# Kernel optimization log

Hardware: AMD Instinct MI355X
Metric: run time of the kernel (lower is better)

Reference implementation:

```python
import jax, jax.numpy as jnp
import numpy as np

N_DST = 50000
NUM_HEAD = 2
LN_EPS = 1e-5


def setup_inputs() -> dict:
    key = jax.random.key(0)
    ks = jax.random.split(key, 12)
    n_dst, n_src, E = 50000, 200000, 250000
    dim_node, dim_edge, dim_time, dim_out = 128, 64, 64, 128
    d_q = dim_node + dim_time            # w_q input dim
    d_k = dim_node + dim_edge + dim_time  # w_k / w_v input dim
    d_o = dim_node + dim_out              # w_out input dim
    f32 = jnp.float32
    return {
        "h": jax.random.normal(ks[0], (n_dst + n_src, dim_node), f32),
        "dt": jax.random.uniform(ks[1], (E,), f32) * 100.0,
        "ef": jax.random.normal(ks[2], (E, dim_edge), f32),
        # TimeEncode: cos(t * w + b), classic TGAT init w = 1/10^linspace(0,9)
        "time_w": (1.0 / 10.0 ** jnp.linspace(0.0, 9.0, dim_time)).astype(f32),
        "time_b": jnp.zeros((dim_time,), f32),
        "wq_w": (jax.random.normal(ks[3], (d_q, dim_out), f32) / np.sqrt(d_q)),
        "wq_b": jnp.zeros((dim_out,), f32),
        "wk_w": (jax.random.normal(ks[4], (d_k, dim_out), f32) / np.sqrt(d_k)),
        "wk_b": jnp.zeros((dim_out,), f32),
        "wv_w": (jax.random.normal(ks[5], (d_k, dim_out), f32) / np.sqrt(d_k)),
        "wv_b": jnp.zeros((dim_out,), f32),
        "wo_w": (jax.random.normal(ks[6], (d_o, dim_out), f32) / np.sqrt(d_o)),
        "wo_b": jnp.zeros((dim_out,), f32),
        "ln_g": jnp.ones((dim_out,), f32),
        "ln_b": jnp.zeros((dim_out,), f32),
        "nbr_idx": jax.random.randint(ks[7], (E,), 0, n_src),
        "edge_dst": jax.random.randint(ks[8], (E,), 0, n_dst),
    }


def reference(h, dt, ef, time_w, time_b, wq_w, wq_b, wk_w, wk_b, wv_w, wv_b,
              wo_w, wo_b, ln_g, ln_b, nbr_idx, edge_dst):
    n_dst = N_DST
    H = NUM_HEAD
    h_dst = h[:n_dst]                       # [n_dst, D]
    h_src = h[n_dst:]                       # [n_src, D]

    # time encoding: cos(t * w + b)
    time_feat = jnp.cos(dt[:, None] * time_w + time_b)          # [E, Dt]
    zero_time = jnp.broadcast_to(jnp.cos(time_b), (n_dst, time_b.shape[0]))

    Q_in = jnp.concatenate([h_dst, zero_time], axis=1)           # [n_dst, D+Dt]
    K_in = jnp.concatenate([h_src[nbr_idx], ef, time_feat], axis=1)  # [E, D+De+Dt]

    Q = (Q_in @ wq_w + wq_b)[edge_dst]      # [E, dim_out] gathered per edge
    K = K_in @ wk_w + wk_b                  # [E, dim_out]
    V = K_in @ wv_w + wv_b                  # [E, dim_out]

    E_ = Q.shape[0]
    Qh = Q.reshape(E_, H, -1)
    Kh = K.reshape(E_, H, -1)
    Vh = V.reshape(E_, H, -1)

    att_raw = jax.nn.leaky_relu(jnp.sum(Qh * Kh, axis=2), 0.2)   # [E, H]

    # edge_softmax: segment softmax over incoming edges of each dst node
    m = jax.ops.segment_max(att_raw, edge_dst, num_segments=n_dst)
    m = jnp.where(jnp.isfinite(m), m, 0.0)  # guard empty segments
    ex = jnp.exp(att_raw - m[edge_dst])
    den = jax.ops.segment_sum(ex, edge_dst, num_segments=n_dst)
    att = ex / den[edge_dst]                # [E, H]

    Vw = (Vh * att[..., None]).reshape(E_, -1)                   # [E, dim_out]
    agg = jax.ops.segment_sum(Vw, edge_dst, num_segments=n_dst)  # [n_dst, dim_out]

    pre = jax.nn.relu(jnp.concatenate([agg, h_dst], axis=1) @ wo_w + wo_b)
    mu = jnp.mean(pre, axis=-1, keepdims=True)
    var = jnp.var(pre, axis=-1, keepdims=True)
    return (pre - mu) / jnp.sqrt(var + LN_EPS) * ln_g + ln_b
```

## Files before the change

### kernel.cpp

```cpp
#include <hip/hip_runtime.h>
#include <hip/hip_bf16.h>
#include <math.h>


using bf16 = __hip_bfloat16;
typedef __attribute__((ext_vector_type(8))) short short8;
typedef __attribute__((ext_vector_type(4))) float f32x4;

static __device__ __forceinline__ unsigned short bf16_bits(float x) {
    bf16 h = __float2bfloat16(x);
    unsigned short b;
    __builtin_memcpy(&b, &h, 2);
    return b;
}
static __device__ __forceinline__ unsigned pk2(float x, float y) {
    return (unsigned)bf16_bits(x) | ((unsigned)bf16_bits(y) << 16);
}
static __device__ __forceinline__ float bflo(unsigned u) {
    return __uint_as_float(u << 16);
}
static __device__ __forceinline__ float bfhi(unsigned u) {
    return __uint_as_float(u & 0xffff0000u);
}
union frag_u { short8 s; unsigned u[4]; };

__global__ void k_pack(unsigned short* wkT, unsigned short* wvT, unsigned short* woT,
                       unsigned short* wqhT, unsigned short* wqlT, float* qbias,
                       const float* __restrict__ wk_w, const float* __restrict__ wv_w,
                       const float* __restrict__ wo_w, const float* __restrict__ wq_w,
                       const float* __restrict__ wq_b, const float* __restrict__ time_b) {
    int idx = blockIdx.x * blockDim.x + threadIdx.x;
    if (idx < 32768) {
        int n = idx >> 8, k = idx & 255;
        wkT[idx] = bf16_bits(wk_w[(size_t)k * 128 + n]);
        wvT[idx] = bf16_bits(wv_w[(size_t)k * 128 + n]);
        woT[idx] = bf16_bits(wo_w[(size_t)k * 128 + n]);
        if (idx < 16384) {
            int n2 = idx >> 7, k2 = idx & 127;
            float v = wq_w[(size_t)k2 * 128 + n2];
            unsigned short hb = bf16_bits(v);
            wqhT[idx] = hb;
            wqlT[idx] = bf16_bits(v - __uint_as_float((unsigned)hb << 16));
        }
        if (idx < 128) {
            float s = wq_b[idx];
            for (int j = 0; j < 64; ++j)
                s += cosf(time_b[j]) * wq_w[(128 + j) * 128 + idx];
            qbias[idx] = s;
        }
    }
}

__global__ void k_count(const int* __restrict__ edst, int* cnt, int E) {
    int e = blockIdx.x * 256 + threadIdx.x;
    if (e < E) atomicAdd(&cnt[edst[e]], 1);
}

__global__ void k_scan1(const int* __restrict__ cnt, int* rs, int* bsum, int n) {
    __shared__ int s[256];
    int t = threadIdx.x;
    int i = blockIdx.x * 256 + t;
    int v = (i < n) ? cnt[i] : 0;
    s[t] = v;
    __syncthreads();
    for (int off = 1; off < 256; off <<= 1) {
        int x = (t >= off) ? s[t - off] : 0;
        __syncthreads();
        s[t] += x;
        __syncthreads();
    }
    if (i < n) rs[i] = s[t] - v;
    if (t == 255) bsum[blockIdx.x] = s[255];
}

__global__ void k_scan2(int* bsum, int nblk) {
    __shared__ int s[256];
    int t = threadIdx.x;
    int v = (t < nblk) ? bsum[t] : 0;
    s[t] = v;
    __syncthreads();
    for (int off = 1; off < 256; off <<= 1) {
        int x = (t >= off) ? s[t - off] : 0;
        __syncthreads();
        s[t] += x;
        __syncthreads();
    }
    if (t < nblk) bsum[t] = s[t] - v;
}

__global__ void k_scatter(const int* __restrict__ edst, const int* __restrict__ rs,
                          const int* __restrict__ bsum, int* fill, int* epos, int E) {
    int e = blockIdx.x * 256 + threadIdx.x;
    if (e < E) {
        int d = edst[e];
        epos[e] = rs[d] + bsum[d >> 8] + atomicAdd(&fill[d], 1);
    }
}

__global__ __launch_bounds__(512) void k_q(
    float* __restrict__ Q, const float* __restrict__ h,
    const unsigned short* __restrict__ wqhT, const unsigned short* __restrict__ wqlT,
    const float* __restrict__ qbias, int ndst)
{
    __shared__ unsigned short Bs[32768];
    int tid = threadIdx.x;
    int lane = tid & 63, l15 = lane & 15, lk = lane >> 4;
    int r0 = blockIdx.x * 128 + (tid >> 6) * 16;
    int ra = r0 + l15;
    int rc = (ra < ndst) ? ra : (ndst - 1);
    const float* hrow = h + (size_t)rc * 128;

    float4 hx[4][2];
    #pragma unroll
    for (int kk = 0; kk < 4; ++kk) {
        int c0 = kk * 32 + lk * 8;
        hx[kk][0] = *reinterpret_cast<const float4*>(hrow + c0);
        hx[kk][1] = *reinterpret_cast<const float4*>(hrow + c0 + 4);
    }

    #pragma unroll
    for (int it = 0; it < 4; ++it) {
        int i = it * 512 + tid;
        int row = i >> 4, c = i & 15;
        int sw = ((c ^ (row & 15)) << 3);
        uint4 v = *reinterpret_cast<const uint4*>(wqhT + (size_t)row * 128 + c * 8);
        *reinterpret_cast<uint4*>(Bs + row * 128 + sw) = v;
        uint4 w = *reinterpret_cast<const uint4*>(wqlT + (size_t)row * 128 + c * 8);
        *reinterpret_cast<uint4*>(Bs + 16384 + row * 128 + sw) = w;
    }

    frag_u ah[4], al[4];
    #pragma unroll
    for (int kk = 0; kk < 4; ++kk) {
        float xs[8] = {hx[kk][0].x, hx[kk][0].y, hx[kk][0].z, hx[kk][0].w,
                       hx[kk][1].x, hx[kk][1].y, hx[kk][1].z, hx[kk][1].w};
        unsigned short hb[8];
        float lo[8];
        #pragma unroll
        for (int t = 0; t < 8; ++t) {
            hb[t] = bf16_bits(xs[t]);
            lo[t] = xs[t] - __uint_as_float((unsigned)hb[t] << 16);
        }
        #pragma unroll
        for (int t = 0; t < 4; ++t)
            ah[kk].u[t] = (unsigned)hb[2*t] | ((unsigned)hb[2*t+1] << 16);
        al[kk].u[0] = pk2(lo[0], lo[1]); al[kk].u[1] = pk2(lo[2], lo[3]);
        al[kk].u[2] = pk2(lo[4], lo[5]); al[kk].u[3] = pk2(lo[6], lo[7]);
    }

    f32x4 ck[8];
    #pragma unroll
    for (int nt = 0; nt < 8; ++nt) ck[nt] = (f32x4){0.f, 0.f, 0.f, 0.f};

    __syncthreads();
    #pragma unroll
    for (int kk2 = 0; kk2 < 4; ++kk2) {
        int co = ((kk2 * 4 + lk) ^ l15) << 3;
        #pragma unroll
        for (int nt = 0; nt < 8; ++nt) {
            int ro = (nt * 16 + l15) * 128;
            short8 bh = *reinterpret_cast<const short8*>(Bs + ro + co);
            short8 bl = *reinterpret_cast<const short8*>(Bs + 16384 + ro + co);
            ck[nt] = __builtin_amdgcn_mfma_f32_16x16x32_bf16(ah[kk2].s, bh, ck[nt], 0, 0, 0);
            ck[nt] = __builtin_amdgcn_mfma_f32_16x16x32_bf16(al[kk2].s, bh, ck[nt], 0, 0, 0);
            ck[nt] = __builtin_amdgcn_mfma_f32_16x16x32_bf16(ah[kk2].s, bl, ck[nt], 0, 0, 0);
        }
    }

    #pragma unroll
    for (int nt = 0; nt < 8; ++nt) {
        int col = nt * 16 + l15;
        float qb = qbias[col];
        #pragma unroll
        for (int j = 0; j < 4; ++j) {
            int row = r0 + lk * 4 + j;
            if (row < ndst) Q[(size_t)row * 128 + col] = ck[nt][j] + qb;
        }
    }
}

__global__ __launch_bounds__(512) void k_kvA(
    const float* __restrict__ h, const int* __restrict__ nbr, const int* __restrict__ edst,
    const float* __restrict__ dt, const float* __restrict__ ef,
    const float* __restrict__ time_w, const float* __restrict__ time_b,
    const unsigned short* __restrict__ wkT, const unsigned short* __restrict__ wvT,
    const float* __restrict__ wk_b, const float* __restrict__ Q,
    const int* __restrict__ epos,
    unsigned short* __restrict__ Vbuf, float2* __restrict__ att2, int ndst, int E)
{
    __shared__ unsigned short Bs[32768];
    int tid  = threadIdx.x;
    int lane = tid & 63;
    int l15  = lane & 15;
    int lk   = lane >> 4;
    int e0   = blockIdx.x * 128 + (tid >> 6) * 16;

    int  ea = e0 + l15;
    bool va = ea < E;
    int  na = va ? nbr[ea] : 0;
    float da = va ? dt[ea] : 0.f;
    const float* hrow = h + (size_t)(ndst + na) * 128;
    const float* erow = ef + (size_t)ea * 64;

    int dstr[4], pe[4];
    bool evv[4];
    #pragma unroll
    for (int j = 0; j < 4; ++j) {
        int ed = e0 + lk * 4 + j;
        evv[j]  = ed < E;
        dstr[j] = evv[j] ? edst[ed] : 0;
        pe[j]   = evv[j] ? epos[ed] : 0;
    }

    float4 hx[4][2], ex_[2][2];
    const float4 z4 = make_float4(0.f, 0.f, 0.f, 0.f);
    #pragma unroll
    for (int kk = 0; kk < 4; ++kk) {
        int c0 = kk * 32 + lk * 8;
        hx[kk][0] = va ? *reinterpret_cast<const float4*>(hrow + c0)     : z4;
        hx[kk][1] = va ? *reinterpret_cast<const float4*>(hrow + c0 + 4) : z4;
    }
    #pragma unroll
    for (int t = 0; t < 2; ++t) {
        int c = (4 + t) * 32 + lk * 8 - 128;
        ex_[t][0] = va ? *reinterpret_cast<const float4*>(erow + c)     : z4;
        ex_[t][1] = va ? *reinterpret_cast<const float4*>(erow + c + 4) : z4;
    }

    float qg[8][4];
    #pragma unroll
    for (int nt = 0; nt < 8; ++nt) {
        int gc = nt * 16 + l15;
        #pragma unroll
        for (int j = 0; j < 4; ++j)
            qg[nt][j] = Q[(size_t)dstr[j] * 128 + gc];
    }

    #pragma unroll
    for (int it = 0; it < 8; ++it) {
        int i = it * 512 + tid;
        int row = i >> 5, c = i & 31;
        uint4 v = *reinterpret_cast<const uint4*>(wkT + (size_t)row * 256 + c * 8);
        *reinterpret_cast<uint4*>(Bs + row * 256 + ((c ^ (row & 15)) << 3)) = v;
    }

    float tf[16];
    {
        int j0 = lk * 8;
        #pragma unroll
        for (int t = 0; t < 8; ++t) tf[t]     = __cosf(fmaf(da, time_w[j0 + t],      time_b[j0 + t]));
        #pragma unroll
        for (int t = 0; t < 8; ++t) tf[8 + t] = __cosf(fmaf(da, time_w[j0 + 32 + t], time_b[j0 + 32 + t]));
    }

    frag_u a[8];
    #pragma unroll
    for (int kk = 0; kk < 4; ++kk) {
        a[kk].u[0] = pk2(hx[kk][0].x, hx[kk][0].y); a[kk].u[1] = pk2(hx[kk][0].z, hx[kk][0].w);
        a[kk].u[2] = pk2(hx[kk][1].x, hx[kk][1].y); a[kk].u[3] = pk2(hx[kk][1].z, hx[kk][1].w);
    }
    #pragma unroll
    for (int t = 0; t < 2; ++t) {
        a[4+t].u[0] = pk2(ex_[t][0].x, ex_[t][0].y); a[4+t].u[1] = pk2(ex_[t][0].z, ex_[t][0].w);
        a[4+t].u[2] = pk2(ex_[t][1].x, ex_[t][1].y); a[4+t].u[3] = pk2(ex_[t][1].z, ex_[t][1].w);
    }
    a[6].u[0] = pk2(tf[0], tf[1]);  a[6].u[1] = pk2(tf[2], tf[3]);
    a[6].u[2] = pk2(tf[4], tf[5]);  a[6].u[3] = pk2(tf[6], tf[7]);
    a[7].u[0] = pk2(tf[8], tf[9]);  a[7].u[1] = pk2(tf[10], tf[11]);
    a[7].u[2] = pk2(tf[12], tf[13]); a[7].u[3] = pk2(tf[14], tf[15]);

    f32x4 ck[8];
    #pragma unroll
    for (int nt = 0; nt < 8; ++nt) ck[nt] = (f32x4){0.f, 0.f, 0.f, 0.f};

    __syncthreads();
    #pragma unroll
    for (int kk2 = 0; kk2 < 8; ++kk2) {
        int co = ((kk2 * 4 + lk) ^ l15) << 3;
        #pragma unroll
        for (int nt = 0; nt < 8; ++nt) {
            short8 b = *reinterpret_cast<const short8*>(Bs + (nt * 16 + l15) * 256 + co);
            ck[nt] = __builtin_amdgcn_mfma_f32_16x16x32_bf16(a[kk2].s, b, ck[nt], 0, 0, 0);
        }
    }
    __syncthreads();
    #pragma unroll
    for (int it = 0; it < 8; ++it) {
        int i = it * 512 + tid;
        int row = i >> 5, c = i & 31;
        uint4 v = *reinterpret_cast<const uint4*>(wvT + (size_t)row * 256 + c * 8);
        *reinterpret_cast<uint4*>(Bs + row * 256 + ((c ^ (row & 15)) << 3)) = v;
    }

    float p0[4], p1[4];
    #pragma unroll
    for (int j = 0; j < 4; ++j) { p0[j] = 0.f; p1[j] = 0.f; }
    #pragma unroll
    for (int nt = 0; nt < 8; ++nt) {
        float kb = wk_b[nt * 16 + l15];
        #pragma unroll
        for (int j = 0; j < 4; ++j) {
            float t = (ck[nt][j] + kb) * qg[nt][j];
            if (nt < 4) p0[j] += t; else p1[j] += t;
        }
    }
    #pragma unroll
    for (int m = 1; m <= 8; m <<= 1)
        #pragma unroll
        for (int j = 0; j < 4; ++j) {
            p0[j] += __shfl_xor(p0[j], m, 64);
            p1[j] += __shfl_xor(p1[j], m, 64);
        }
    if (l15 == 0) {
        #pragma unroll
        for (int j = 0; j < 4; ++j)
            if (evv[j]) {
                float r0 = p0[j]; r0 = (r0 >= 0.f) ? r0 : 0.2f * r0;
                float r1 = p1[j]; r1 = (r1 >= 0.f) ? r1 : 0.2f * r1;
                att2[pe[j]] = make_float2(r0, r1);
            }
    }

    f32x4 cv[8];
    #pragma unroll
    for (int nt = 0; nt < 8; ++nt) cv[nt] = (f32x4){0.f, 0.f, 0.f, 0.f};
    __syncthreads();
    #pragma unroll
    for (int kk2 = 0; kk2 < 8; ++kk2) {
        int co = ((kk2 * 4 + lk) ^ l15) << 3;
        #pragma unroll
        for (int nt = 0; nt < 8; ++nt) {
            short8 b = *reinterpret_cast<const short8*>(Bs + (nt * 16 + l15) * 256 + co);
            cv[nt] = __builtin_amdgcn_mfma_f32_16x16x32_bf16(a[kk2].s, b, cv[nt], 0, 0, 0);
        }
    }

    #pragma unroll
    for (int j = 0; j < 4; ++j)
        if (evv[j]) {
            uint4 val;
            val.x = pk2(cv[0][j], cv[1][j]);
            val.y = pk2(cv[2][j], cv[3][j]);
            val.z = pk2(cv[4][j], cv[5][j]);
            val.w = pk2(cv[6][j], cv[7][j]);
            *reinterpret_cast<uint4*>(Vbuf + (size_t)pe[j] * 128 + l15 * 8) = val;
        }
}

__global__ __launch_bounds__(256) void k_agg(
    const unsigned short* __restrict__ Vbuf, const float2* __restrict__ att2,
    const int* __restrict__ rs, const int* __restrict__ bsum, const int* __restrict__ cnt,
    const float* __restrict__ wv_b, float* __restrict__ agg, int ndst)
{
    int w = threadIdx.x >> 6, lane = threadIdx.x & 63;
    int d = blockIdx.x * 4 + w;
    if (d >= ndst) return;
    int p0 = lane * 2, p1 = p0 + 1;
    int c0 = ((p0 & 7) << 4) + (p0 >> 3);
    int c1 = ((p1 & 7) << 4) + (p1 >> 3);
    bool h0 = (p0 & 4) != 0, h1 = (p1 & 4) != 0;
    int base = rs[d] + bsum[d >> 8], n = cnt[d];
    const unsigned* V32 = reinterpret_cast<const unsigned*>(Vbuf);
    float den0 = 0.f, den1 = 0.f, acc0 = 0.f, acc1 = 0.f;
    int i = 0;
    for (; i + 4 <= n; i += 4) {
        size_t r = (size_t)(base + i);
        float2 a0 = att2[r], a1 = att2[r+1], a2 = att2[r+2], a3 = att2[r+3];
        unsigned w0 = V32[r*64 + lane], w1 = V32[(r+1)*64 + lane];
        unsigned w2 = V32[(r+2)*64 + lane], w3 = V32[(r+3)*64 + lane];
        float e00 = __expf(a0.x), e01 = __expf(a0.y);
        float e10 = __expf(a1.x), e11 = __expf(a1.y);
        float e20 = __expf(a2.x), e21 = __expf(a2.y);
        float e30 = __expf(a3.x), e31 = __expf(a3.y);
        den0 += e00 + e10 + e20 + e30;
        den1 += e01 + e11 + e21 + e31;
        acc0 = fmaf(h0 ? e01 : e00, bflo(w0), acc0);
        acc1 = fmaf(h1 ? e01 : e00, bfhi(w0), acc1);
        acc0 = fmaf(h0 ? e11 : e10, bflo(w1), acc0);
        acc1 = fmaf(h1 ? e11 : e10, bfhi(w1), acc1);
        acc0 = fmaf(h0 ? e21 : e20, bflo(w2), acc0);
        acc1 = fmaf(h1 ? e21 : e20, bfhi(w2), acc1);
        acc0 = fmaf(h0 ? e31 : e30, bflo(w3), acc0);
        acc1 = fmaf(h1 ? e31 : e30, bfhi(w3), acc1);
    }
    for (; i < n; ++i) {
        size_t r = (size_t)(base + i);
        float2 at = att2[r];
        float ex0 = __expf(at.x), ex1 = __expf(at.y);
        den0 += ex0; den1 += ex1;
        unsigned vv = V32[r*64 + lane];
        acc0 = fmaf(h0 ? ex1 : ex0, bflo(vv), acc0);
        acc1 = fmaf(h1 ? ex1 : ex0, bfhi(vv), acc1);
    }
    float o0 = 0.f, o1 = 0.f;
    if (n > 0) {
        o0 = acc0 / (h0 ? den1 : den0) + wv_b[c0];
        o1 = acc1 / (h1 ? den1 : den0) + wv_b[c1];
    }
    agg[(size_t)d * 128 + c0] = o0;
    agg[(size_t)d * 128 + c1] = o1;
}

__global__ __launch_bounds__(512) void k_out(
    const float* __restrict__ agg, const float* __restrict__ h,
    const unsigned short* __restrict__ woT, const float* __restrict__ wo_b,
    const float* __restrict__ ln_g, const float* __restrict__ ln_b,
    float* __restrict__ out, int ndst)
{
    __shared__ unsigned short Bs[32768];
    int tid = threadIdx.x;
    int lane = tid & 63, l15 = lane & 15, lk = lane >> 4;
    int r0 = blockIdx.x * 128 + (tid >> 6) * 16;
    int ra = r0 + l15;
    int rc = (ra < ndst) ? ra : (ndst - 1);
    const float* arow = agg + (size_t)rc * 128;
    const float* hrow = h + (size_t)rc * 128;

    float4 ax[4][2], hx[4][2];
    #pragma unroll
    for (int kk = 0; kk < 4; ++kk) {
        int c0 = kk * 32 + lk * 8;
        ax[kk][0] = *reinterpret_cast<const float4*>(arow + c0);
        ax[kk][1] = *reinterpret_cast<const float4*>(arow + c0 + 4);
        hx[kk][0] = *reinterpret_cast<const float4*>(hrow + c0);
        hx[kk][1] = *reinterpret_cast<const float4*>(hrow + c0 + 4);
    }

    #pragma unroll
    for (int it = 0; it < 8; ++it) {
        int i = it * 512 + tid;
        int row = i >> 5, c = i & 31;
        uint4 v = *reinterpret_cast<const uint4*>(woT + (size_t)row * 256 + c * 8);
        *reinterpret_cast<uint4*>(Bs + row * 256 + ((c ^ (row & 15)) << 3)) = v;
    }

    frag_u aa[4], ah[4];
    #pragma unroll
    for (int kk = 0; kk < 4; ++kk) {
        aa[kk].u[0] = pk2(ax[kk][0].x, ax[kk][0].y); aa[kk].u[1] = pk2(ax[kk][0].z, ax[kk][0].w);
        aa[kk].u[2] = pk2(ax[kk][1].x, ax[kk][1].y); aa[kk].u[3] = pk2(ax[kk][1].z, ax[kk][1].w);
        ah[kk].u[0] = pk2(hx[kk][0].x, hx[kk][0].y); ah[kk].u[1] = pk2(hx[kk][0].z, hx[kk][0].w);
        ah[kk].u[2] = pk2(hx[kk][1].x, hx[kk][1].y); ah[kk].u[3] = pk2(hx[kk][1].z, hx[kk][1].w);
    }

    f32x4 ck[8];
    #pragma unroll
    for (int nt = 0; nt < 8; ++nt) ck[nt] = (f32x4){0.f, 0.f, 0.f, 0.f};

    __syncthreads();
    #pragma unroll
    for (int kk2 = 0; kk2 < 4; ++kk2) {
        int coA = ((kk2 * 4 + lk) ^ l15) << 3;
        int coH = (((16 + kk2 * 4 + lk)) ^ l15) << 3;
        #pragma unroll
        for (int nt = 0; nt < 8; ++nt) {
            int ro = (nt * 16 + l15) * 256;
            short8 bA = *reinterpret_cast<const short8*>(Bs + ro + coA);
            short8 bH = *reinterpret_cast<const short8*>(Bs + ro + coH);
            ck[nt] = __builtin_amdgcn_mfma_f32_16x16x32_bf16(aa[kk2].s, bA, ck[nt], 0, 0, 0);
            ck[nt] = __builtin_amdgcn_mfma_f32_16x16x32_bf16(ah[kk2].s, bH, ck[nt], 0, 0, 0);
        }
    }

    #pragma unroll
    for (int nt = 0; nt < 8; ++nt) {
        float bo = wo_b[nt * 16 + l15];
        #pragma unroll
        for (int j = 0; j < 4; ++j)
            ck[nt][j] = fmaxf(ck[nt][j] + bo, 0.f);
    }
    float s1[4], s2[4];
    #pragma unroll
    for (int j = 0; j < 4; ++j) { s1[j] = 0.f; s2[j] = 0.f; }
    #pragma unroll
    for (int nt = 0; nt < 8; ++nt)
        #pragma unroll
        for (int j = 0; j < 4; ++j) {
            s1[j] += ck[nt][j];
            s2[j] = fmaf(ck[nt][j], ck[nt][j], s2[j]);
        }
    #pragma unroll
    for (int m = 1; m <= 8; m <<= 1)
        #pragma unroll
        for (int j = 0; j < 4; ++j) {
            s1[j] += __shfl_xor(s1[j], m, 64);
            s2[j] += __shfl_xor(s2[j], m, 64);
        }
    float mean[4], rstd[4];
    #pragma unroll
    for (int j = 0; j < 4; ++j) {
        mean[j] = s1[j] * (1.f / 128.f);
        float var = s2[j] * (1.f / 128.f) - mean[j] * mean[j];
        rstd[j] = rsqrtf(var + 1e-5f);
    }
    #pragma unroll
    for (int nt = 0; nt < 8; ++nt) {
        int col = nt * 16 + l15;
        float g = ln_g[col], lb = ln_b[col];
        #pragma unroll
        for (int j = 0; j < 4; ++j) {
            int row = r0 + lk * 4 + j;
            if (row < ndst)
                out[(size_t)row * 128 + col] = (ck[nt][j] - mean[j]) * rstd[j] * g + lb;
        }
    }
}

extern "C" void kernel_launch(void* const* d_in, const int* in_sizes, int n_in,
                              void* d_out, int out_size, void* d_ws, size_t ws_size,
                              hipStream_t stream) {
    const float* h      = (const float*)d_in[0];
    const float* dt     = (const float*)d_in[1];
    const float* ef     = (const float*)d_in[2];
    const float* time_w = (const float*)d_in[3];
    const float* time_b = (const float*)d_in[4];
    const float* wq_w   = (const float*)d_in[5];
    const float* wq_b   = (const float*)d_in[6];
    const float* wk_w   = (const float*)d_in[7];
    const float* wk_b   = (const float*)d_in[8];
    const float* wv_w   = (const float*)d_in[9];
    const float* wv_b   = (const float*)d_in[10];
    const float* wo_w   = (const float*)d_in[11];
    const float* wo_b   = (const float*)d_in[12];
    const float* ln_g   = (const float*)d_in[13];
    const float* ln_b   = (const float*)d_in[14];
    const int* nbr      = (const int*)d_in[15];
    const int* edst     = (const int*)d_in[16];

    int E    = in_sizes[1];
    int ndst = out_size / 128;
    int nblk = (ndst + 255) / 256;

    char* wsb = (char*)d_ws;
    float* qbias = (float*)wsb;                 wsb += 512;
    float* Q     = (float*)wsb;                 wsb += (size_t)ndst * 128 * 4;
    float* agg   = (float*)wsb;                 wsb += (size_t)ndst * 128 * 4;
    unsigned short* wkT  = (unsigned short*)wsb; wsb += 32768 * 2;
    unsigned short* wvT  = (unsigned short*)wsb; wsb += 32768 * 2;
    unsigned short* woT  = (unsigned short*)wsb; wsb += 32768 * 2;
    unsigned short* wqhT = (unsigned short*)wsb; wsb += 16384 * 2;
    unsigned short* wqlT = (unsigned short*)wsb; wsb += 16384 * 2;
    int* cnt    = (int*)wsb;                    wsb += (size_t)ndst * 4;
    int* fill   = (int*)wsb;                    wsb += (size_t)ndst * 4;
    int* rs     = (int*)wsb;                    wsb += (size_t)ndst * 4;
    int* bsum   = (int*)wsb;                    wsb += 1024;
    int* epos   = (int*)wsb;                    wsb += (size_t)E * 4;
    float2* att2 = (float2*)wsb;                wsb += (size_t)E * 8;
    unsigned short* Vbuf = (unsigned short*)wsb; wsb += (size_t)E * 128 * 2;

    hipMemsetAsync(cnt, 0, (size_t)ndst * 8, stream);
    k_pack<<<128, 256, 0, stream>>>(wkT, wvT, woT, wqhT, wqlT, qbias,
                                    wk_w, wv_w, wo_w, wq_w, wq_b, time_b);
    k_count<<<(E + 255) / 256, 256, 0, stream>>>(edst, cnt, E);
    k_scan1<<<nblk, 256, 0, stream>>>(cnt, rs, bsum, ndst);
    k_scan2<<<1, 256, 0, stream>>>(bsum, nblk);
    k_scatter<<<(E + 255) / 256, 256, 0, stream>>>(edst, rs, bsum, fill, epos, E);
    k_q<<<(ndst + 127) / 128, 512, 0, stream>>>(Q, h, wqhT, wqlT, qbias, ndst);
    k_kvA<<<(E + 127) / 128, 512, 0, stream>>>(h, nbr, edst, dt, ef, time_w, time_b,
                                               wkT, wvT, wk_b, Q, epos, Vbuf, att2, ndst, E);
    k_agg<<<(ndst + 3) / 4, 256, 0, stream>>>(Vbuf, att2, rs, bsum, cnt, wv_b, agg, ndst);
    k_out<<<(ndst + 127) / 128, 512, 0, stream>>>(agg, h, woT, wo_b, ln_g, ln_b,
                                                  (float*)d_out, ndst);
}
```

Before: 247.8 us.

## Make KV kernel persistent with both weights resident, store agg in bf16

The K/V projection kernel becomes a persistent grid of 256 blocks with 1024 threads. Each block loads both the K and V weight matrices into 128KB of shared memory once and then loops over 256-edge tiles. This removes the per-block weight reload and the mid-kernel syncs between the K and V passes. The aggregated features are also written as bf16 instead of fp32, which halves that intermediate traffic and drops a conversion in the output kernel. The costs are lower occupancy from the large shared-memory footprint and 1024-thread blocks, and a grid fixed at 256 blocks, which may not fill the device evenly.

```diff
diff --git a/kernel.cpp b/kernel.cpp
--- a/kernel.cpp
+++ b/kernel.cpp
@@ -122,11 +122,11 @@
     for (int it = 0; it < 4; ++it) {
         int i = it * 512 + tid;
         int row = i >> 4, c = i & 15;
-        int sw = ((c ^ (row & 15)) << 3);
-        uint4 v = *reinterpret_cast<const uint4*>(wqhT + (size_t)row * 128 + c * 8);
-        *reinterpret_cast<uint4*>(Bs + row * 128 + sw) = v;
-        uint4 w = *reinterpret_cast<const uint4*>(wqlT + (size_t)row * 128 + c * 8);
-        *reinterpret_cast<uint4*>(Bs + 16384 + row * 128 + sw) = w;
+        int sw = row * 128 + ((c ^ (row & 15)) << 3);
+        *reinterpret_cast<uint4*>(Bs + sw) =
+            *reinterpret_cast<const uint4*>(wqhT + (size_t)row * 128 + c * 8);
+        *reinterpret_cast<uint4*>(Bs + 16384 + sw) =
+            *reinterpret_cast<const uint4*>(wqlT + (size_t)row * 128 + c * 8);
     }
 
     frag_u ah[4], al[4];
@@ -179,178 +179,176 @@
     }
 }
 
-__global__ __launch_bounds__(512) void k_kvA(
+__global__ __launch_bounds__(1024) void k_kvA(
     const float* __restrict__ h, const int* __restrict__ nbr, const int* __restrict__ edst,
     const float* __restrict__ dt, const float* __restrict__ ef,
     const float* __restrict__ time_w, const float* __restrict__ time_b,
     const unsigned short* __restrict__ wkT, const unsigned short* __restrict__ wvT,
     const float* __restrict__ wk_b, const float* __restrict__ Q,
     const int* __restrict__ epos,
-    unsigned short* __restrict__ Vbuf, float2* __restrict__ att2, int ndst, int E)
+    unsigned short* __restrict__ Vbuf, float2* __restrict__ att2,
+    int ndst, int E, int ntiles)
 {
-    __shared__ unsigned short Bs[32768];
+    __shared__ unsigned short Bs[65536];
     int tid  = threadIdx.x;
     int lane = tid & 63;
     int l15  = lane & 15;
     int lk   = lane >> 4;
-    int e0   = blockIdx.x * 128 + (tid >> 6) * 16;
-
-    int  ea = e0 + l15;
-    bool va = ea < E;
-    int  na = va ? nbr[ea] : 0;
-    float da = va ? dt[ea] : 0.f;
-    const float* hrow = h + (size_t)(ndst + na) * 128;
-    const float* erow = ef + (size_t)ea * 64;
-
-    int dstr[4], pe[4];
-    bool evv[4];
-    #pragma unroll
-    for (int j = 0; j < 4; ++j) {
-        int ed = e0 + lk * 4 + j;
-        evv[j]  = ed < E;
-        dstr[j] = evv[j] ? edst[ed] : 0;
-        pe[j]   = evv[j] ? epos[ed] : 0;
-    }
-
-    float4 hx[4][2], ex_[2][2];
-    const float4 z4 = make_float4(0.f, 0.f, 0.f, 0.f);
-    #pragma unroll
-    for (int kk = 0; kk < 4; ++kk) {
-        int c0 = kk * 32 + lk * 8;
-        hx[kk][0] = va ? *reinterpret_cast<const float4*>(hrow + c0)     : z4;
-        hx[kk][1] = va ? *reinterpret_cast<const float4*>(hrow + c0 + 4) : z4;
-    }
-    #pragma unroll
-    for (int t = 0; t < 2; ++t) {
-        int c = (4 + t) * 32 + lk * 8 - 128;
-        ex_[t][0] = va ? *reinterpret_cast<const float4*>(erow + c)     : z4;
-        ex_[t][1] = va ? *reinterpret_cast<const float4*>(erow + c + 4) : z4;
-    }
-
-    float qg[8][4];
-    #pragma unroll
-    for (int nt = 0; nt < 8; ++nt) {
-        int gc = nt * 16 + l15;
-        #pragma unroll
-        for (int j = 0; j < 4; ++j)
-            qg[nt][j] = Q[(size_t)dstr[j] * 128 + gc];
-    }
 
     #pragma unroll
     for (int it = 0; it < 8; ++it) {
-        int i = it * 512 + tid;
-        int row = i >> 5, c = i & 31;
-        uint4 v = *reinterpret_cast<const uint4*>(wkT + (size_t)row * 256 + c * 8);
-        *reinterpret_cast<uint4*>(Bs + row * 256 + ((c ^ (row & 15)) << 3)) = v;
-    }
-
-    float tf[16];
-    {
-        int j0 = lk * 8;
-        #pragma unroll
-        for (int t = 0; t < 8; ++t) tf[t]     = __cosf(fmaf(da, time_w[j0 + t],      time_b[j0 + t]));
-        #pragma unroll
-        for (int t = 0; t < 8; ++t) tf[8 + t] = __cosf(fmaf(da, time_w[j0 + 32 + t], time_b[j0 + 32 + t]));
-    }
-
-    frag_u a[8];
-    #pragma unroll
-    for (int kk = 0; kk < 4; ++kk) {
-        a[kk].u[0] = pk2(hx[kk][0].x, hx[kk][0].y); a[kk].u[1] = pk2(hx[kk][0].z, hx[kk][0].w);
-        a[kk].u[2] = pk2(hx[kk][1].x, hx[kk][1].y); a[kk].u[3] = pk2(hx[kk][1].z, hx[kk][1].w);
-    }
-    #pragma unroll
-    for (int t = 0; t < 2; ++t) {
-        a[4+t].u[0] = pk2(ex_[t][0].x, ex_[t][0].y); a[4+t].u[1] = pk2(ex_[t][0].z, ex_[t][0].w);
-        a[4+t].u[2] = pk2(ex_[t][1].x, ex_[t][1].y); a[4+t].u[3] = pk2(ex_[t][1].z, ex_[t][1].w);
-    }
-    a[6].u[0] = pk2(tf[0], tf[1]);  a[6].u[1] = pk2(tf[2], tf[3]);
-    a[6].u[2] = pk2(tf[4], tf[5]);  a[6].u[3] = pk2(tf[6], tf[7]);
-    a[7].u[0] = pk2(tf[8], tf[9]);  a[7].u[1] = pk2(tf[10], tf[11]);
-    a[7].u[2] = pk2(tf[12], tf[13]); a[7].u[3] = pk2(tf[14], tf[15]);
-
-    f32x4 ck[8];
-    #pragma unroll
-    for (int nt = 0; nt < 8; ++nt) ck[nt] = (f32x4){0.f, 0.f, 0.f, 0.f};
-
+        int i = it * 1024 + tid;
+        int tb  = i >> 12;
+        int row = (i >> 5) & 127;
+        int c   = i & 31;
+        const unsigned short* src = tb ? wvT : wkT;
+        *reinterpret_cast<uint4*>(Bs + tb * 32768 + row * 256 + ((c ^ (row & 15)) << 3)) =
+            *reinterpret_cast<const uint4*>(src + (size_t)row * 256 + c * 8);
+    }
+    float kb[8];
+    #pragma unroll
+    for (int nt = 0; nt < 8; ++nt) kb[nt] = wk_b[nt * 16 + l15];
     __syncthreads();
-    #pragma unroll
-    for (int kk2 = 0; kk2 < 8; ++kk2) {
-        int co = ((kk2 * 4 + lk) ^ l15) << 3;
+
+    for (int tile = blockIdx.x; tile < ntiles; tile += gridDim.x) {
+        int e0 = tile * 256 + (tid >> 6) * 16;
+
+        int  ea = e0 + l15;
+        bool va = ea < E;
+        int  na = va ? nbr[ea] : 0;
+        float da = va ? dt[ea] : 0.f;
+        const float* hrow = h + (size_t)(ndst + na) * 128;
+        const float* erow = ef + (size_t)ea * 64;
+
+        int dstr[4], pe[4];
+        bool evv[4];
+        #pragma unroll
+        for (int j = 0; j < 4; ++j) {
+            int ed = e0 + lk * 4 + j;
+            evv[j]  = ed < E;
+            dstr[j] = evv[j] ? edst[ed] : 0;
+            pe[j]   = evv[j] ? epos[ed] : 0;
+        }
+
+        float4 hx[4][2], ex_[2][2];
+        const float4 z4 = make_float4(0.f, 0.f, 0.f, 0.f);
+        #pragma unroll
+        for (int kk = 0; kk < 4; ++kk) {
+            int c0 = kk * 32 + lk * 8;
+            hx[kk][0] = va ? *reinterpret_cast<const float4*>(hrow + c0)     : z4;
+            hx[kk][1] = va ? *reinterpret_cast<const float4*>(hrow + c0 + 4) : z4;
+        }
+        #pragma unroll
+        for (int t = 0; t < 2; ++t) {
+            int c = (4 + t) * 32 + lk * 8 - 128;
+            ex_[t][0] = va ? *reinterpret_cast<const float4*>(erow + c)     : z4;
+            ex_[t][1] = va ? *reinterpret_cast<const float4*>(erow + c + 4) : z4;
+        }
+
+        float qg[8][4];
         #pragma unroll
         for (int nt = 0; nt < 8; ++nt) {
-            short8 b = *reinterpret_cast<const short8*>(Bs + (nt * 16 + l15) * 256 + co);
-            ck[nt] = __builtin_amdgcn_mfma_f32_16x16x32_bf16(a[kk2].s, b, ck[nt], 0, 0, 0);
-        }
-    }
-    __syncthreads();
-    #pragma unroll
-    for (int it = 0; it < 8; ++it) {
-        int i = it * 512 + tid;
-        int row = i >> 5, c = i & 31;
-        uint4 v = *reinterpret_cast<const uint4*>(wvT + (size_t)row * 256 + c * 8);
-        *reinterpret_cast<uint4*>(Bs + row * 256 + ((c ^ (row & 15)) << 3)) = v;
-    }
-
-    float p0[4], p1[4];
-    #pragma unroll
-    for (int j = 0; j < 4; ++j) { p0[j] = 0.f; p1[j] = 0.f; }
-    #pragma unroll
-    for (int nt = 0; nt < 8; ++nt) {
-        float kb = wk_b[nt * 16 + l15];
-        #pragma unroll
-        for (int j = 0; j < 4; ++j) {
-            float t = (ck[nt][j] + kb) * qg[nt][j];
-            if (nt < 4) p0[j] += t; else p1[j] += t;
-        }
-    }
-    #pragma unroll
-    for (int m = 1; m <= 8; m <<= 1)
-        #pragma unroll
-        for (int j = 0; j < 4; ++j) {
-            p0[j] += __shfl_xor(p0[j], m, 64);
-            p1[j] += __shfl_xor(p1[j], m, 64);
-        }
-    if (l15 == 0) {
+            int gc = nt * 16 + l15;
+            #pragma unroll
+            for (int j = 0; j < 4; ++j)
+                qg[nt][j] = Q[(size_t)dstr[j] * 128 + gc];
+        }
+
+        float tf[16];
+        {
+            int j0 = lk * 8;
+            #pragma unroll
+            for (int t = 0; t < 8; ++t) tf[t]     = __cosf(fmaf(da, time_w[j0 + t],      time_b[j0 + t]));
+            #pragma unroll
+            for (int t = 0; t < 8; ++t) tf[8 + t] = __cosf(fmaf(da, time_w[j0 + 32 + t], time_b[j0 + 32 + t]));
+        }
+
+        frag_u a[8];
+        #pragma unroll
+        for (int kk = 0; kk < 4; ++kk) {
+            a[kk].u[0] = pk2(hx[kk][0].x, hx[kk][0].y); a[kk].u[1] = pk2(hx[kk][0].z, hx[kk][0].w);
+            a[kk].u[2] = pk2(hx[kk][1].x, hx[kk][1].y); a[kk].u[3] = pk2(hx[kk][1].z, hx[kk][1].w);
+        }
+        #pragma unroll
+        for (int t = 0; t < 2; ++t) {
+            a[4+t].u[0] = pk2(ex_[t][0].x, ex_[t][0].y); a[4+t].u[1] = pk2(ex_[t][0].z, ex_[t][0].w);
+            a[4+t].u[2] = pk2(ex_[t][1].x, ex_[t][1].y); a[4+t].u[3] = pk2(ex_[t][1].z, ex_[t][1].w);
+        }
+        a[6].u[0] = pk2(tf[0], tf[1]);  a[6].u[1] = pk2(tf[2], tf[3]);
+        a[6].u[2] = pk2(tf[4], tf[5]);  a[6].u[3] = pk2(tf[6], tf[7]);
+        a[7].u[0] = pk2(tf[8], tf[9]);  a[7].u[1] = pk2(tf[10], tf[11]);
+        a[7].u[2] = pk2(tf[12], tf[13]); a[7].u[3] = pk2(tf[14], tf[15]);
+
+        f32x4 ck[8];
+        #pragma unroll
+        for (int nt = 0; nt < 8; ++nt) ck[nt] = (f32x4){0.f, 0.f, 0.f, 0.f};
+        #pragma unroll
+        for (int kk2 = 0; kk2 < 8; ++kk2) {
+            int co = ((kk2 * 4 + lk) ^ l15) << 3;
+            #pragma unroll
+            for (int nt = 0; nt < 8; ++nt) {
+                short8 b = *reinterpret_cast<const short8*>(Bs + (nt * 16 + l15) * 256 + co);
+                ck[nt] = __builtin_amdgcn_mfma_f32_16x16x32_bf16(a[kk2].s, b, ck[nt], 0, 0, 0);
+            }
+        }
+
+        float p0[4], p1[4];
+        #pragma unroll
+        for (int j = 0; j < 4; ++j) { p0[j] = 0.f; p1[j] = 0.f; }
+        #pragma unroll
+        for (int nt = 0; nt < 8; ++nt)
+            #pragma unroll
+            for (int j = 0; j < 4; ++j) {
+                float t = (ck[nt][j] + kb[nt]) * qg[nt][j];
+                if (nt < 4) p0[j] += t; else p1[j] += t;
+            }
+        #pragma unroll
+        for (int m = 1; m <= 8; m <<= 1)
+            #pragma unroll
+            for (int j = 0; j < 4; ++j) {
+                p0[j] += __shfl_xor(p0[j], m, 64);
+                p1[j] += __shfl_xor(p1[j], m, 64);
+            }
+        if (l15 == 0) {
+            #pragma unroll
+            for (int j = 0; j < 4; ++j)
+                if (evv[j]) {
+                    float r0 = p0[j]; r0 = (r0 >= 0.f) ? r0 : 0.2f * r0;
+                    float r1 = p1[j]; r1 = (r1 >= 0.f) ? r1 : 0.2f * r1;
+                    att2[pe[j]] = make_float2(r0, r1);
+                }
+        }
+
+        f32x4 cv[8];
+        #pragma unroll
+        for (int nt = 0; nt < 8; ++nt) cv[nt] = (f32x4){0.f, 0.f, 0.f, 0.f};
+        #pragma unroll
+        for (int kk2 = 0; kk2 < 8; ++kk2) {
+            int co = ((kk2 * 4 + lk) ^ l15) << 3;
+            #pragma unroll
+            for (int nt = 0; nt < 8; ++nt) {
+                short8 b = *reinterpret_cast<const short8*>(Bs + 32768 + (nt * 16 + l15) * 256 + co);
+                cv[nt] = __builtin_amdgcn_mfma_f32_16x16x32_bf16(a[kk2].s, b, cv[nt], 0, 0, 0);
+            }
+        }
+
         #pragma unroll
         for (int j = 0; j < 4; ++j)
             if (evv[j]) {
-                float r0 = p0[j]; r0 = (r0 >= 0.f) ? r0 : 0.2f * r0;
-                float r1 = p1[j]; r1 = (r1 >= 0.f) ? r1 : 0.2f * r1;
-                att2[pe[j]] = make_float2(r0, r1);
+                uint4 val;
+                val.x = pk2(cv[0][j], cv[1][j]);
+                val.y = pk2(cv[2][j], cv[3][j]);
+                val.z = pk2(cv[4][j], cv[5][j]);
+                val.w = pk2(cv[6][j], cv[7][j]);
+                *reinterpret_cast<uint4*>(Vbuf + (size_t)pe[j] * 128 + l15 * 8) = val;
             }
     }
-
-    f32x4 cv[8];
-    #pragma unroll
-    for (int nt = 0; nt < 8; ++nt) cv[nt] = (f32x4){0.f, 0.f, 0.f, 0.f};
-    __syncthreads();
-    #pragma unroll
-    for (int kk2 = 0; kk2 < 8; ++kk2) {
-        int co = ((kk2 * 4 + lk) ^ l15) << 3;
-        #pragma unroll
-        for (int nt = 0; nt < 8; ++nt) {
-            short8 b = *reinterpret_cast<const short8*>(Bs + (nt * 16 + l15) * 256 + co);
-            cv[nt] = __builtin_amdgcn_mfma_f32_16x16x32_bf16(a[kk2].s, b, cv[nt], 0, 0, 0);
-        }
-    }
-
-    #pragma unroll
-    for (int j = 0; j < 4; ++j)
-        if (evv[j]) {
-            uint4 val;
-            val.x = pk2(cv[0][j], cv[1][j]);
-            val.y = pk2(cv[2][j], cv[3][j]);
-            val.z = pk2(cv[4][j], cv[5][j]);
-            val.w = pk2(cv[6][j], cv[7][j]);
-            *reinterpret_cast<uint4*>(Vbuf + (size_t)pe[j] * 128 + l15 * 8) = val;
-        }
 }
 
 __global__ __launch_bounds__(256) void k_agg(
     const unsigned short* __restrict__ Vbuf, const float2* __restrict__ att2,
     const int* __restrict__ rs, const int* __restrict__ bsum, const int* __restrict__ cnt,
-    const float* __restrict__ wv_b, float* __restrict__ agg, int ndst)
+    const float* __restrict__ wv_b, unsigned short* __restrict__ agg16, int ndst)
 {
     int w = threadIdx.x >> 6, lane = threadIdx.x & 63;
     int d = blockIdx.x * 4 + w;
@@ -397,12 +395,12 @@
         o0 = acc0 / (h0 ? den1 : den0) + wv_b[c0];
         o1 = acc1 / (h1 ? den1 : den0) + wv_b[c1];
     }
-    agg[(size_t)d * 128 + c0] = o0;
-    agg[(size_t)d * 128 + c1] = o1;
+    agg16[(size_t)d * 128 + c0] = bf16_bits(o0);
+    agg16[(size_t)d * 128 + c1] = bf16_bits(o1);
 }
 
 __global__ __launch_bounds__(512) void k_out(
-    const float* __restrict__ agg, const float* __restrict__ h,
+    const unsigned short* __restrict__ agg16, const float* __restrict__ h,
     const unsigned short* __restrict__ woT, const float* __restrict__ wo_b,
     const float* __restrict__ ln_g, const float* __restrict__ ln_b,
     float* __restrict__ out, int ndst)
@@ -413,15 +411,15 @@
     int r0 = blockIdx.x * 128 + (tid >> 6) * 16;
     int ra = r0 + l15;
     int rc = (ra < ndst) ? ra : (ndst - 1);
-    const float* arow = agg + (size_t)rc * 128;
+    const unsigned short* arow = agg16 + (size_t)rc * 128;
     const float* hrow = h + (size_t)rc * 128;
 
-    float4 ax[4][2], hx[4][2];
+    frag_u aa[4];
+    float4 hx[4][2];
     #pragma unroll
     for (int kk = 0; kk < 4; ++kk) {
         int c0 = kk * 32 + lk * 8;
-        ax[kk][0] = *reinterpret_cast<const float4*>(arow + c0);
-        ax[kk][1] = *reinterpret_cast<const float4*>(arow + c0 + 4);
+        aa[kk].s = *reinterpret_cast<const short8*>(arow + c0);
         hx[kk][0] = *reinterpret_cast<const float4*>(hrow + c0);
         hx[kk][1] = *reinterpret_cast<const float4*>(hrow + c0 + 4);
     }
@@ -434,11 +432,9 @@
         *reinterpret_cast<uint4*>(Bs + row * 256 + ((c ^ (row & 15)) << 3)) = v;
     }
 
-    frag_u aa[4], ah[4];
+    frag_u ah[4];
     #pragma unroll
     for (int kk = 0; kk < 4; ++kk) {
-        aa[kk].u[0] = pk2(ax[kk][0].x, ax[kk][0].y); aa[kk].u[1] = pk2(ax[kk][0].z, ax[kk][0].w);
-        aa[kk].u[2] = pk2(ax[kk][1].x, ax[kk][1].y); aa[kk].u[3] = pk2(ax[kk][1].z, ax[kk][1].w);
         ah[kk].u[0] = pk2(hx[kk][0].x, hx[kk][0].y); ah[kk].u[1] = pk2(hx[kk][0].z, hx[kk][0].w);
         ah[kk].u[2] = pk2(hx[kk][1].x, hx[kk][1].y); ah[kk].u[3] = pk2(hx[kk][1].z, hx[kk][1].w);
     }
@@ -530,11 +526,12 @@
     int E    = in_sizes[1];
     int ndst = out_size / 128;
     int nblk = (ndst + 255) / 256;
+    int ntiles = (E + 255) / 256;
 
     char* wsb = (char*)d_ws;
     float* qbias = (float*)wsb;                 wsb += 512;
     float* Q     = (float*)wsb;                 wsb += (size_t)ndst * 128 * 4;
-    float* agg   = (float*)wsb;                 wsb += (size_t)ndst * 128 * 4;
+    unsigned short* agg16 = (unsigned short*)wsb; wsb += (size_t)ndst * 128 * 2;
     unsigned short* wkT  = (unsigned short*)wsb; wsb += 32768 * 2;
     unsigned short* wvT  = (unsigned short*)wsb; wsb += 32768 * 2;
     unsigned short* woT  = (unsigned short*)wsb; wsb += 32768 * 2;
@@ -556,9 +553,10 @@
     k_scan2<<<1, 256, 0, stream>>>(bsum, nblk);
     k_scatter<<<(E + 255) / 256, 256, 0, stream>>>(edst, rs, bsum, fill, epos, E);
     k_q<<<(ndst + 127) / 128, 512, 0, stream>>>(Q, h, wqhT, wqlT, qbias, ndst);
-    k_kvA<<<(E + 127) / 128, 512, 0, stream>>>(h, nbr, edst, dt, ef, time_w, time_b,
-                                               wkT, wvT, wk_b, Q, epos, Vbuf, att2, ndst, E);
-    k_agg<<<(ndst + 3) / 4, 256, 0, stream>>>(Vbuf, att2, rs, bsum, cnt, wv_b, agg, ndst);
-    k_out<<<(ndst + 127) / 128, 512, 0, stream>>>(agg, h, woT, wo_b, ln_g, ln_b,
+    k_kvA<<<256, 1024, 0, stream>>>(h, nbr, edst, dt, ef, time_w, time_b,
+                                    wkT, wvT, wk_b, Q, epos, Vbuf, att2,
+                                    ndst, E, ntiles);
+    k_agg<<<(ndst + 3) / 4, 256, 0, stream>>>(Vbuf, att2, rs, bsum, cnt, wv_b, agg16, ndst);
+    k_out<<<(ndst + 127) / 128, 512, 0, stream>>>(agg16, h, woT, wo_b, ln_g, ln_b,
                                                   (float*)d_out, ndst);
 }
```

Measured after the change: 844.1 us. +240.6%, slower.
